# Performance work log

Hardware: AMD Instinct MI355X
Metric: run time of the kernel (lower is better)

The kernel has to match this reference:

```python
import jax, jax.numpy as jnp
import numpy as np


def setup_inputs() -> dict:
    key = jax.random.key(0)
    kx, kq, kb, kc = jax.random.split(key, 4)
    N, D = 16384, 1024
    x = jax.random.normal(kx, (N, D), dtype=jnp.float32)
    Q = jax.random.normal(kq, (D, D), dtype=jnp.float32)
    b = jax.random.normal(kb, (D,), dtype=jnp.float32)
    c = jax.random.normal(kc, (1,), dtype=jnp.float32)
    return {"x": x, "Q": Q, "b": b, "c": c}


def reference(x, Q, b, c):
    # y_i = x_i^T Q x_i + b^T x_i + c  (same math as diag(x @ Q @ x.T)
    # without materializing the NxN matrix)
    xQ = x @ Q                                # [N, D]
    quad = jnp.sum(xQ * x, axis=-1)           # [N]
    y = quad + x @ b + c                       # [N] (c broadcasts from [1])
    return y[:, None]                          # [N, 1]
```

## Files before the change

kernel.cpp:

```cpp
#include <hip/hip_runtime.h>
#include <hip/hip_bf16.h>


#define DD 1024
#define KH 256
#define KSTEP 8
#define NTT 32
#define LDS_ROW 264

typedef short v8s __attribute__((ext_vector_type(8)));
typedef float v4f __attribute__((ext_vector_type(4)));

__device__ __forceinline__ short f2b(float f) {
    union { __hip_bfloat16 h; short s; } u;
    u.h = __float2bfloat16(f);
    return u.s;
}

__global__ __launch_bounds__(512, 2)
void quad_kernel(const float* __restrict__ x, const float* __restrict__ Q,
                 const float* __restrict__ bvec, const float* __restrict__ cptr,
                 float* __restrict__ y)
{
    __shared__ short lq[2][16 * LDS_ROW];

    const int tid  = threadIdx.x;
    const int lane = tid & 63;
    const int wave = tid >> 6;
    const int quad = lane >> 4;
    const int l15  = lane & 15;

    const int seg  = blockIdx.x & 7;
    const int rblk = blockIdx.x >> 3;
    const int kq   = seg >> 1;
    const int cs   = seg & 1;

    const int row_base = rblk * 512 + wave * 64;
    const int kofs  = kq * KH;
    const int tbase = cs * NTT;

    v8s a[4][KSTEP];
    #pragma unroll
    for (int g = 0; g < 4; ++g) {
        const float* xr = x + (size_t)(row_base + g * 16 + l15) * DD + kofs + quad * 8;
        #pragma unroll
        for (int s = 0; s < KSTEP; ++s) {
            const float4 f0 = *(const float4*)(xr + s * 32);
            const float4 f1 = *(const float4*)(xr + s * 32 + 4);
            v8s t;
            t[0]=f2b(f0.x); t[1]=f2b(f0.y); t[2]=f2b(f0.z); t[3]=f2b(f0.w);
            t[4]=f2b(f1.x); t[5]=f2b(f1.y); t[6]=f2b(f1.z); t[7]=f2b(f1.w);
            a[g][s] = t;
            asm volatile("" : "+a"(a[g][s]));
        }
    }

    int s_nn[2], s_k4[2];
    #pragma unroll
    for (int i = 0; i < 2; ++i) {
        const int idx = tid + i * 512;
        s_nn[i] = idx >> 6;
        s_k4[i] = idx & 63;
    }

    float4 pf[2];
    #pragma unroll
    for (int i = 0; i < 2; ++i)
        pf[i] = *(const float4*)(Q + (size_t)(tbase * 16 + s_nn[i]) * DD + kofs + s_k4[i] * 4);

    float acc[4][4];
    #pragma unroll
    for (int g = 0; g < 4; ++g)
        #pragma unroll
        for (int r = 0; r < 4; ++r) acc[g][r] = 0.f;

    for (int t = 0; t < NTT; ++t) {
        const int tg = tbase + t;

        short* dst = &lq[t & 1][0];
        #pragma unroll
        for (int i = 0; i < 2; ++i) {
            const float4 f = pf[i];
            short4 s;
            s.x=f2b(f.x); s.y=f2b(f.y); s.z=f2b(f.z); s.w=f2b(f.w);
            *(short4*)&dst[s_nn[i] * LDS_ROW + s_k4[i] * 4] = s;
        }
        __syncthreads();

        if (t + 1 < NTT) {
            #pragma unroll
            for (int i = 0; i < 2; ++i)
                pf[i] = *(const float4*)(Q + (size_t)((tg + 1) * 16 + s_nn[i]) * DD + kofs + s_k4[i] * 4);
        }

        const int n = tg * 16 + l15;
        const float bn = (kq == 0) ? bvec[n] : 0.f;
        float xv[4][4];
        {
            const float* xc = x + (size_t)(row_base + quad * 4) * DD + n;
            #pragma unroll
            for (int g = 0; g < 4; ++g)
                #pragma unroll
                for (int r = 0; r < 4; ++r)
                    xv[g][r] = xc[(size_t)(g * 16 + r) * DD];
        }

        v4f cf[4];
        #pragma unroll
        for (int g = 0; g < 4; ++g) cf[g] = (v4f){0.f, 0.f, 0.f, 0.f};
        const short* bp = &lq[t & 1][l15 * LDS_ROW + quad * 8];
        #pragma unroll
        for (int s = 0; s < KSTEP; ++s) {
            const v8s bfrag = *(const v8s*)(bp + s * 32);
            #pragma unroll
            for (int g = 0; g < 4; ++g)
                cf[g] = __builtin_amdgcn_mfma_f32_16x16x32_bf16(a[g][s], bfrag, cf[g], 0, 0, 0);
        }

        #pragma unroll
        for (int g = 0; g < 4; ++g)
            #pragma unroll
            for (int r = 0; r < 4; ++r)
                acc[g][r] += (cf[g][r] + bn) * xv[g][r];
    }

    const float cc = (seg == 0) ? cptr[0] : 0.f;
    #pragma unroll
    for (int g = 0; g < 4; ++g) {
        #pragma unroll
        for (int r = 0; r < 4; ++r) {
            float v = acc[g][r];
            v += __shfl_xor(v, 1); v += __shfl_xor(v, 2);
            v += __shfl_xor(v, 4); v += __shfl_xor(v, 8);
            if (l15 == 0)
                atomicAdd(&y[row_base + g * 16 + quad * 4 + r], v + cc);
        }
    }
}

extern "C" void kernel_launch(void* const* d_in, const int* in_sizes, int n_in,
                              void* d_out, int out_size, void* d_ws, size_t ws_size,
                              hipStream_t stream)
{
    const float* x = (const float*)d_in[0];
    const float* Q = (const float*)d_in[1];
    const float* b = (const float*)d_in[2];
    const float* c = (const float*)d_in[3];
    float* y = (float*)d_out;

    hipMemsetAsync(y, 0, (size_t)out_size * sizeof(float), stream);
    quad_kernel<<<dim3(256), dim3(512), 0, stream>>>(x, Q, b, c, y);
}
```

Measured before the change: 155.2 us.

## Reshape block tile to 256 rows by 32 columns per round, doubling grid

Each wave now covers 32 rows instead of 64, and each round stages 32 columns of Q into LDS instead of 16, with two B fragments per k-step. The grid doubles to 512 blocks so the 256 CUs get more blocks, and the number of barrier rounds per block halves. The register footprint for the x fragments shrinks while LDS per block doubles. In exchange, Q traffic per output row rises because each block serves fewer rows.

```diff
diff --git a/kernel.cpp b/kernel.cpp
--- a/kernel.cpp
+++ b/kernel.cpp
@@ -5,7 +5,7 @@
 #define DD 1024
 #define KH 256
 #define KSTEP 8
-#define NTT 32
+#define NROUND 16
 #define LDS_ROW 264
 
 typedef short v8s __attribute__((ext_vector_type(8)));
@@ -22,7 +22,7 @@
                  const float* __restrict__ bvec, const float* __restrict__ cptr,
                  float* __restrict__ y)
 {
-    __shared__ short lq[2][16 * LDS_ROW];
+    __shared__ short lq[2][32 * LDS_ROW];
 
     const int tid  = threadIdx.x;
     const int lane = tid & 63;
@@ -35,13 +35,13 @@
     const int kq   = seg >> 1;
     const int cs   = seg & 1;
 
-    const int row_base = rblk * 512 + wave * 64;
-    const int kofs  = kq * KH;
-    const int tbase = cs * NTT;
+    const int row_base = rblk * 256 + wave * 32;
+    const int kofs     = kq * KH;
+    const int col_base = cs * 512;
 
-    v8s a[4][KSTEP];
+    v8s a[2][KSTEP];
     #pragma unroll
-    for (int g = 0; g < 4; ++g) {
+    for (int g = 0; g < 2; ++g) {
         const float* xr = x + (size_t)(row_base + g * 16 + l15) * DD + kofs + quad * 8;
         #pragma unroll
         for (int s = 0; s < KSTEP; ++s) {
@@ -55,31 +55,29 @@
         }
     }
 
-    int s_nn[2], s_k4[2];
+    int s_nn[4], s_k4[4];
     #pragma unroll
-    for (int i = 0; i < 2; ++i) {
+    for (int i = 0; i < 4; ++i) {
         const int idx = tid + i * 512;
         s_nn[i] = idx >> 6;
         s_k4[i] = idx & 63;
     }
 
-    float4 pf[2];
+    float4 pf[4];
     #pragma unroll
-    for (int i = 0; i < 2; ++i)
-        pf[i] = *(const float4*)(Q + (size_t)(tbase * 16 + s_nn[i]) * DD + kofs + s_k4[i] * 4);
+    for (int i = 0; i < 4; ++i)
+        pf[i] = *(const float4*)(Q + (size_t)(col_base + s_nn[i]) * DD + kofs + s_k4[i] * 4);
 
-    float acc[4][4];
+    float acc[2][4];
     #pragma unroll
-    for (int g = 0; g < 4; ++g)
+    for (int g = 0; g < 2; ++g)
         #pragma unroll
         for (int r = 0; r < 4; ++r) acc[g][r] = 0.f;
 
-    for (int t = 0; t < NTT; ++t) {
-        const int tg = tbase + t;
-
+    for (int t = 0; t < NROUND; ++t) {
         short* dst = &lq[t & 1][0];
         #pragma unroll
-        for (int i = 0; i < 2; ++i) {
+        for (int i = 0; i < 4; ++i) {
             const float4 f = pf[i];
             short4 s;
             s.x=f2b(f.x); s.y=f2b(f.y); s.z=f2b(f.z); s.w=f2b(f.w);
@@ -87,46 +85,55 @@
         }
         __syncthreads();
 
-        if (t + 1 < NTT) {
+        if (t + 1 < NROUND) {
             #pragma unroll
-            for (int i = 0; i < 2; ++i)
-                pf[i] = *(const float4*)(Q + (size_t)((tg + 1) * 16 + s_nn[i]) * DD + kofs + s_k4[i] * 4);
+            for (int i = 0; i < 4; ++i)
+                pf[i] = *(const float4*)(Q + (size_t)(col_base + (t + 1) * 32 + s_nn[i]) * DD + kofs + s_k4[i] * 4);
         }
 
-        const int n = tg * 16 + l15;
-        const float bn = (kq == 0) ? bvec[n] : 0.f;
-        float xv[4][4];
+        const int n0 = col_base + t * 32 + l15;
+        const float bn0 = (kq == 0) ? bvec[n0]      : 0.f;
+        const float bn1 = (kq == 0) ? bvec[n0 + 16] : 0.f;
+        float xv[2][2][4];
         {
-            const float* xc = x + (size_t)(row_base + quad * 4) * DD + n;
+            const float* xc = x + (size_t)(row_base + quad * 4) * DD + n0;
             #pragma unroll
-            for (int g = 0; g < 4; ++g)
+            for (int nt = 0; nt < 2; ++nt)
                 #pragma unroll
-                for (int r = 0; r < 4; ++r)
-                    xv[g][r] = xc[(size_t)(g * 16 + r) * DD];
+                for (int g = 0; g < 2; ++g)
+                    #pragma unroll
+                    for (int r = 0; r < 4; ++r)
+                        xv[nt][g][r] = xc[(size_t)(g * 16 + r) * DD + nt * 16];
         }
 
-        v4f cf[4];
+        v4f cf[2][2];
         #pragma unroll
-        for (int g = 0; g < 4; ++g) cf[g] = (v4f){0.f, 0.f, 0.f, 0.f};
+        for (int nt = 0; nt < 2; ++nt)
+            #pragma unroll
+            for (int g = 0; g < 2; ++g) cf[nt][g] = (v4f){0.f, 0.f, 0.f, 0.f};
         const short* bp = &lq[t & 1][l15 * LDS_ROW + quad * 8];
         #pragma unroll
         for (int s = 0; s < KSTEP; ++s) {
-            const v8s bfrag = *(const v8s*)(bp + s * 32);
+            const v8s b0 = *(const v8s*)(bp + s * 32);
+            const v8s b1 = *(const v8s*)(bp + 16 * LDS_ROW + s * 32);
             #pragma unroll
-            for (int g = 0; g < 4; ++g)
-                cf[g] = __builtin_amdgcn_mfma_f32_16x16x32_bf16(a[g][s], bfrag, cf[g], 0, 0, 0);
+            for (int g = 0; g < 2; ++g) {
+                cf[0][g] = __builtin_amdgcn_mfma_f32_16x16x32_bf16(a[g][s], b0, cf[0][g], 0, 0, 0);
+                cf[1][g] = __builtin_amdgcn_mfma_f32_16x16x32_bf16(a[g][s], b1, cf[1][g], 0, 0, 0);
+            }
         }
 
         #pragma unroll
-        for (int g = 0; g < 4; ++g)
+        for (int g = 0; g < 2; ++g)
             #pragma unroll
             for (int r = 0; r < 4; ++r)
-                acc[g][r] += (cf[g][r] + bn) * xv[g][r];
+                acc[g][r] += (cf[0][g][r] + bn0) * xv[0][g][r]
+                           + (cf[1][g][r] + bn1) * xv[1][g][r];
     }
 
     const float cc = (seg == 0) ? cptr[0] : 0.f;
     #pragma unroll
-    for (int g = 0; g < 4; ++g) {
+    for (int g = 0; g < 2; ++g) {
         #pragma unroll
         for (int r = 0; r < 4; ++r) {
             float v = acc[g][r];
@@ -149,5 +156,5 @@
     float* y = (float*)d_out;
 
     hipMemsetAsync(y, 0, (size_t)out_size * sizeof(float), stream);
-    quad_kernel<<<dim3(256), dim3(512), 0, stream>>>(x, Q, b, c, y);
+    quad_kernel<<<dim3(512), dim3(512), 0, stream>>>(x, Q, b, c, y);
 }
```

After: 152.4 us. Within noise of the previous version (-1.8%).

## Restructure to 32-row blocks with in-block K split and LDS reduction

Applied to the files above, without the earlier changes.

Each block now handles 32 rows across all of K. Its 8 waves split the work as 2 row groups by 4 K quarters, and partial MFMA results are reduced through shared memory instead of global atomics, which also removes the memset. The x values used in the epilogue come from the bf16 copies already held in registers and staged into LDS, replacing strided global loads, at some precision cost. The trade-off is two block barriers per column tile and every block streaming all of Q, which raises Q traffic per block.

```diff
diff --git a/kernel.cpp b/kernel.cpp
--- a/kernel.cpp
+++ b/kernel.cpp
@@ -3,10 +3,8 @@
 
 
 #define DD 1024
-#define KH 256
-#define KSTEP 8
-#define NTT 32
-#define LDS_ROW 264
+#define TROW 2064
+#define XROW 272
 
 typedef short v8s __attribute__((ext_vector_type(8)));
 typedef float v4f __attribute__((ext_vector_type(4)));
@@ -17,125 +15,120 @@
     return u.s;
 }
 
-__global__ __launch_bounds__(512, 2)
+__global__ __launch_bounds__(512, 4)
 void quad_kernel(const float* __restrict__ x, const float* __restrict__ Q,
                  const float* __restrict__ bvec, const float* __restrict__ cptr,
                  float* __restrict__ y)
 {
-    __shared__ short lq[2][16 * LDS_ROW];
+    __shared__ __align__(16) char  tile[16 * TROW];
+    __shared__ float parts[2][4][16][16];
+    __shared__ __align__(16) short xvb[2][32][XROW];
 
     const int tid  = threadIdx.x;
     const int lane = tid & 63;
     const int wave = tid >> 6;
     const int quad = lane >> 4;
     const int l15  = lane & 15;
+    const int kq   = wave & 3;
+    const int rg   = wave >> 2;
 
-    const int seg  = blockIdx.x & 7;
-    const int rblk = blockIdx.x >> 3;
-    const int kq   = seg >> 1;
-    const int cs   = seg & 1;
+    const int row_base = blockIdx.x * 32;
 
-    const int row_base = rblk * 512 + wave * 64;
-    const int kofs  = kq * KH;
-    const int tbase = cs * NTT;
+    const int sn = tid >> 8;
+    const int sk = tid & 255;
 
-    v8s a[4][KSTEP];
+    float4 pf[8];
     #pragma unroll
-    for (int g = 0; g < 4; ++g) {
-        const float* xr = x + (size_t)(row_base + g * 16 + l15) * DD + kofs + quad * 8;
+    for (int i = 0; i < 8; ++i)
+        pf[i] = *(const float4*)(Q + (size_t)(sn + 2 * i) * DD + sk * 4);
+
+    v8s a[8];
+    {
+        const float* xr = x + (size_t)(row_base + rg * 16 + l15) * DD + kq * 256 + quad * 8;
         #pragma unroll
-        for (int s = 0; s < KSTEP; ++s) {
+        for (int s = 0; s < 8; ++s) {
             const float4 f0 = *(const float4*)(xr + s * 32);
             const float4 f1 = *(const float4*)(xr + s * 32 + 4);
             v8s t;
             t[0]=f2b(f0.x); t[1]=f2b(f0.y); t[2]=f2b(f0.z); t[3]=f2b(f0.w);
             t[4]=f2b(f1.x); t[5]=f2b(f1.y); t[6]=f2b(f1.z); t[7]=f2b(f1.w);
-            a[g][s] = t;
-            asm volatile("" : "+a"(a[g][s]));
+            a[s] = t;
+            asm volatile("" : "+a"(a[s]));
         }
     }
 
-    int s_nn[2], s_k4[2];
-    #pragma unroll
-    for (int i = 0; i < 2; ++i) {
-        const int idx = tid + i * 512;
-        s_nn[i] = idx >> 6;
-        s_k4[i] = idx & 63;
+    if (kq == 0) {
+        char* d = (char*)&xvb[0][rg * 16 + l15][0] + quad * 16;
+        #pragma unroll
+        for (int s = 0; s < 8; ++s) *(v8s*)(d + s * 64) = a[s];
     }
 
-    float4 pf[2];
     #pragma unroll
-    for (int i = 0; i < 2; ++i)
-        pf[i] = *(const float4*)(Q + (size_t)(tbase * 16 + s_nn[i]) * DD + kofs + s_k4[i] * 4);
+    for (int i = 0; i < 8; ++i) {
+        const float4 f = pf[i];
+        short4 s4; s4.x=f2b(f.x); s4.y=f2b(f.y); s4.z=f2b(f.z); s4.w=f2b(f.w);
+        *(short4*)(tile + (sn + 2 * i) * TROW + sk * 8) = s4;
+    }
+    #pragma unroll
+    for (int i = 0; i < 8; ++i)
+        pf[i] = *(const float4*)(Q + (size_t)(16 + sn + 2 * i) * DD + sk * 4);
 
-    float acc[4][4];
-    #pragma unroll
-    for (int g = 0; g < 4; ++g)
+    __syncthreads();
+
+    const char* bp = tile + l15 * TROW + kq * 512 + quad * 16;
+    float* pw = &parts[rg][kq][quad * 4][0] + l15;
+    const int m = tid >> 4;
+    const int c = tid & 15;
+    const float* pr = &parts[m >> 4][0][m & 15][c];
+
+    float acc = 0.f;
+
+    for (int t = 0; t < 64; ++t) {
+        const float bb = bvec[t * 16 + c];
+
+        v4f cf = (v4f){0.f, 0.f, 0.f, 0.f};
         #pragma unroll
-        for (int r = 0; r < 4; ++r) acc[g][r] = 0.f;
+        for (int s = 0; s < 8; ++s) {
+            const v8s bf = *(const v8s*)(bp + s * 64);
+            cf = __builtin_amdgcn_mfma_f32_16x16x32_bf16(a[s], bf, cf, 0, 0, 0);
+        }
+        #pragma unroll
+        for (int r = 0; r < 4; ++r) pw[r * 16] = cf[r];
 
-    for (int t = 0; t < NTT; ++t) {
-        const int tg = tbase + t;
-
-        short* dst = &lq[t & 1][0];
-        #pragma unroll
-        for (int i = 0; i < 2; ++i) {
-            const float4 f = pf[i];
-            short4 s;
-            s.x=f2b(f.x); s.y=f2b(f.y); s.z=f2b(f.z); s.w=f2b(f.w);
-            *(short4*)&dst[s_nn[i] * LDS_ROW + s_k4[i] * 4] = s;
-        }
         __syncthreads();
 
-        if (t + 1 < NTT) {
+        if (t < 63) {
             #pragma unroll
-            for (int i = 0; i < 2; ++i)
-                pf[i] = *(const float4*)(Q + (size_t)((tg + 1) * 16 + s_nn[i]) * DD + kofs + s_k4[i] * 4);
+            for (int i = 0; i < 8; ++i) {
+                const float4 f = pf[i];
+                short4 s4; s4.x=f2b(f.x); s4.y=f2b(f.y); s4.z=f2b(f.z); s4.w=f2b(f.w);
+                *(short4*)(tile + (sn + 2 * i) * TROW + sk * 8) = s4;
+            }
+            if (t < 62) {
+                #pragma unroll
+                for (int i = 0; i < 8; ++i)
+                    pf[i] = *(const float4*)(Q + (size_t)((t + 2) * 16 + sn + 2 * i) * DD + sk * 4);
+            }
+        }
+        if ((t & 15) == 15 && t < 48 && kq == (t >> 4) + 1) {
+            char* d = (char*)&xvb[((t >> 4) + 1) & 1][rg * 16 + l15][0] + quad * 16;
+            #pragma unroll
+            for (int s = 0; s < 8; ++s) *(v8s*)(d + s * 64) = a[s];
         }
 
-        const int n = tg * 16 + l15;
-        const float bn = (kq == 0) ? bvec[n] : 0.f;
-        float xv[4][4];
-        {
-            const float* xc = x + (size_t)(row_base + quad * 4) * DD + n;
-            #pragma unroll
-            for (int g = 0; g < 4; ++g)
-                #pragma unroll
-                for (int r = 0; r < 4; ++r)
-                    xv[g][r] = xc[(size_t)(g * 16 + r) * DD];
-        }
+        const float cs = pr[0] + pr[256] + pr[512] + pr[768];
+        const int xo = ((t >> 4) & 1) * (32 * XROW) + m * XROW + (t & 15) * 16 + c;
+        union { unsigned u; float f; } uu;
+        uu.u = ((unsigned)(unsigned short)((const short*)xvb)[xo]) << 16;
+        acc += (cs + bb) * uu.f;
 
-        v4f cf[4];
-        #pragma unroll
-        for (int g = 0; g < 4; ++g) cf[g] = (v4f){0.f, 0.f, 0.f, 0.f};
-        const short* bp = &lq[t & 1][l15 * LDS_ROW + quad * 8];
-        #pragma unroll
-        for (int s = 0; s < KSTEP; ++s) {
-            const v8s bfrag = *(const v8s*)(bp + s * 32);
-            #pragma unroll
-            for (int g = 0; g < 4; ++g)
-                cf[g] = __builtin_amdgcn_mfma_f32_16x16x32_bf16(a[g][s], bfrag, cf[g], 0, 0, 0);
-        }
-
-        #pragma unroll
-        for (int g = 0; g < 4; ++g)
-            #pragma unroll
-            for (int r = 0; r < 4; ++r)
-                acc[g][r] += (cf[g][r] + bn) * xv[g][r];
+        __syncthreads();
     }
 
-    const float cc = (seg == 0) ? cptr[0] : 0.f;
-    #pragma unroll
-    for (int g = 0; g < 4; ++g) {
-        #pragma unroll
-        for (int r = 0; r < 4; ++r) {
-            float v = acc[g][r];
-            v += __shfl_xor(v, 1); v += __shfl_xor(v, 2);
-            v += __shfl_xor(v, 4); v += __shfl_xor(v, 8);
-            if (l15 == 0)
-                atomicAdd(&y[row_base + g * 16 + quad * 4 + r], v + cc);
-        }
-    }
+    float v = acc;
+    v += __shfl_xor(v, 1); v += __shfl_xor(v, 2);
+    v += __shfl_xor(v, 4); v += __shfl_xor(v, 8);
+    if (c == 0) y[row_base + m] = v + cptr[0];
 }
 
 extern "C" void kernel_launch(void* const* d_in, const int* in_sizes, int n_in,
@@ -148,6 +141,5 @@
     const float* c = (const float*)d_in[3];
     float* y = (float*)d_out;
 
-    hipMemsetAsync(y, 0, (size_t)out_size * sizeof(float), stream);
-    quad_kernel<<<dim3(256), dim3(512), 0, stream>>>(x, Q, b, c, y);
+    quad_kernel<<<dim3(512), dim3(512), 0, stream>>>(x, Q, b, c, y);
 }
```

Result: slower. 195.6 us (+26.0%).

## Pre-convert Q to bf16, split K across waves, and read x values from LDS

Applied to the files above, without the earlier changes.

A separate kernel now converts Q to bf16 into the workspace. The main kernel gives each block 64 rows, with each of its 8 waves owning a 128-wide K slice. Q fragments are read straight from global memory with a register double buffer, replacing the LDS staging path. Each wave writes its bf16 x fragments back to LDS as float, so the x·(xQ) dot no longer needs strided global loads. A final LDS reduction across waves replaces the memset and atomics, at the cost of an extra launch, a workspace buffer, and x values that are now bf16-rounded in the dot product.

```diff
diff --git a/kernel.cpp b/kernel.cpp
--- a/kernel.cpp
+++ b/kernel.cpp
@@ -3,10 +3,8 @@
 
 
 #define DD 1024
-#define KH 256
-#define KSTEP 8
-#define NTT 32
-#define LDS_ROW 264
+#define XSTRIDE 132
+#define XPHASE (64 * XSTRIDE)
 
 typedef short v8s __attribute__((ext_vector_type(8)));
 typedef float v4f __attribute__((ext_vector_type(4)));
@@ -16,13 +14,66 @@
     u.h = __float2bfloat16(f);
     return u.s;
 }
+__device__ __forceinline__ float b2f(short s) {
+    union { unsigned u; float f; } uu;
+    uu.u = ((unsigned)(unsigned short)s) << 16;
+    return uu.f;
+}
+
+__global__ __launch_bounds__(256, 4)
+void cvt_kernel(const float* __restrict__ Q, short* __restrict__ qb)
+{
+    const int idx = (blockIdx.x * 256 + threadIdx.x) * 4;
+    const float4 f = *(const float4*)(Q + idx);
+    short4 s4;
+    s4.x = f2b(f.x); s4.y = f2b(f.y); s4.z = f2b(f.z); s4.w = f2b(f.w);
+    *(short4*)(qb + idx) = s4;
+}
+
+#define MFMA16(A, B, C) __builtin_amdgcn_mfma_f32_16x16x32_bf16(A, B, C, 0, 0, 0)
+
+#define DUMP_XV()                                                         \
+  { _Pragma("unroll")                                                     \
+    for (int g = 0; g < 4; ++g) {                                         \
+      _Pragma("unroll")                                                   \
+      for (int s = 0; s < 4; ++s) {                                       \
+        float* d = &xvb[wave & 1][(g * 16 + l15) * XSTRIDE + s * 32 + quad * 8]; \
+        const v8s fr = a[g][s];                                           \
+        float4 lo, hi;                                                    \
+        lo.x = b2f(fr[0]); lo.y = b2f(fr[1]); lo.z = b2f(fr[2]); lo.w = b2f(fr[3]); \
+        hi.x = b2f(fr[4]); hi.y = b2f(fr[5]); hi.z = b2f(fr[6]); hi.w = b2f(fr[7]); \
+        *(float4*)d = lo; *((float4*)d + 1) = hi;                         \
+      } } }
+
+#define ROUND(BR, T)                                                      \
+  { v4f cf0 = (v4f){0,0,0,0}, cf1 = (v4f){0,0,0,0};                       \
+    v4f cf2 = (v4f){0,0,0,0}, cf3 = (v4f){0,0,0,0};                       \
+    _Pragma("unroll")                                                     \
+    for (int s = 0; s < 4; ++s) {                                         \
+      cf0 = MFMA16(a[0][s], BR[s], cf0);                                  \
+      cf1 = MFMA16(a[1][s], BR[s], cf1);                                  \
+      cf2 = MFMA16(a[2][s], BR[s], cf2);                                  \
+      cf3 = MFMA16(a[3][s], BR[s], cf3);                                  \
+    }                                                                     \
+    const float* xp = xq + ((((T) >> 3) & 1) * XPHASE) + (((T) & 7) * 16); \
+    const float bb = (wave == 0) ? bvec[(T) * 16 + l15] : 0.f;            \
+    _Pragma("unroll")                                                     \
+    for (int g = 0; g < 4; ++g) {                                         \
+      const v4f cfg = (g == 0) ? cf0 : ((g == 1) ? cf1 : ((g == 2) ? cf2 : cf3)); \
+      _Pragma("unroll")                                                   \
+      for (int r = 0; r < 4; ++r) {                                       \
+        const float xv = xp[(g * 16 + r) * XSTRIDE];                      \
+        acc[g][r] += cfg[r] * xv;                                         \
+        if (wave == 0) acc[g][r] += bb * xv;                              \
+      } } }
 
 __global__ __launch_bounds__(512, 2)
-void quad_kernel(const float* __restrict__ x, const float* __restrict__ Q,
+void quad_kernel(const float* __restrict__ x, const short* __restrict__ qb,
                  const float* __restrict__ bvec, const float* __restrict__ cptr,
                  float* __restrict__ y)
 {
-    __shared__ short lq[2][16 * LDS_ROW];
+    __shared__ __align__(16) float xvb[2][XPHASE];
+    __shared__ float yred[8][64];
 
     const int tid  = threadIdx.x;
     const int lane = tid & 63;
@@ -30,21 +81,20 @@
     const int quad = lane >> 4;
     const int l15  = lane & 15;
 
-    const int seg  = blockIdx.x & 7;
-    const int rblk = blockIdx.x >> 3;
-    const int kq   = seg >> 1;
-    const int cs   = seg & 1;
+    const int row_base = blockIdx.x * 64;
+    const int kb = wave * 128;
 
-    const int row_base = rblk * 512 + wave * 64;
-    const int kofs  = kq * KH;
-    const int tbase = cs * NTT;
+    const short* qp = qb + (size_t)l15 * DD + kb + quad * 8;
+    v8s bA[4], bB[4];
+    #pragma unroll
+    for (int s = 0; s < 4; ++s) bA[s] = *(const v8s*)(qp + s * 32);
 
-    v8s a[4][KSTEP];
+    v8s a[4][4];
     #pragma unroll
     for (int g = 0; g < 4; ++g) {
-        const float* xr = x + (size_t)(row_base + g * 16 + l15) * DD + kofs + quad * 8;
+        const float* xr = x + (size_t)(row_base + g * 16 + l15) * DD + kb + quad * 8;
         #pragma unroll
-        for (int s = 0; s < KSTEP; ++s) {
+        for (int s = 0; s < 4; ++s) {
             const float4 f0 = *(const float4*)(xr + s * 32);
             const float4 f1 = *(const float4*)(xr + s * 32 + 4);
             v8s t;
@@ -55,18 +105,8 @@
         }
     }
 
-    int s_nn[2], s_k4[2];
-    #pragma unroll
-    for (int i = 0; i < 2; ++i) {
-        const int idx = tid + i * 512;
-        s_nn[i] = idx >> 6;
-        s_k4[i] = idx & 63;
-    }
-
-    float4 pf[2];
-    #pragma unroll
-    for (int i = 0; i < 2; ++i)
-        pf[i] = *(const float4*)(Q + (size_t)(tbase * 16 + s_nn[i]) * DD + kofs + s_k4[i] * 4);
+    if (wave == 0) DUMP_XV();
+    __syncthreads();
 
     float acc[4][4];
     #pragma unroll
@@ -74,67 +114,40 @@
         #pragma unroll
         for (int r = 0; r < 4; ++r) acc[g][r] = 0.f;
 
-    for (int t = 0; t < NTT; ++t) {
-        const int tg = tbase + t;
+    const float* xq = &xvb[0][0] + quad * 4 * XSTRIDE + l15;
 
-        short* dst = &lq[t & 1][0];
+    for (int t = 0; t < 64; t += 2) {
+        if ((t & 7) == 0) {
+            if (t) __syncthreads();
+            if (wave == (t >> 3) + 1) DUMP_XV();
+        }
+        qp += 16 * DD;
         #pragma unroll
-        for (int i = 0; i < 2; ++i) {
-            const float4 f = pf[i];
-            short4 s;
-            s.x=f2b(f.x); s.y=f2b(f.y); s.z=f2b(f.z); s.w=f2b(f.w);
-            *(short4*)&dst[s_nn[i] * LDS_ROW + s_k4[i] * 4] = s;
+        for (int s = 0; s < 4; ++s) bB[s] = *(const v8s*)(qp + s * 32);
+        ROUND(bA, t);
+        qp += 16 * DD;
+        if (t + 2 < 64) {
+            #pragma unroll
+            for (int s = 0; s < 4; ++s) bA[s] = *(const v8s*)(qp + s * 32);
         }
-        __syncthreads();
-
-        if (t + 1 < NTT) {
-            #pragma unroll
-            for (int i = 0; i < 2; ++i)
-                pf[i] = *(const float4*)(Q + (size_t)((tg + 1) * 16 + s_nn[i]) * DD + kofs + s_k4[i] * 4);
-        }
-
-        const int n = tg * 16 + l15;
-        const float bn = (kq == 0) ? bvec[n] : 0.f;
-        float xv[4][4];
-        {
-            const float* xc = x + (size_t)(row_base + quad * 4) * DD + n;
-            #pragma unroll
-            for (int g = 0; g < 4; ++g)
-                #pragma unroll
-                for (int r = 0; r < 4; ++r)
-                    xv[g][r] = xc[(size_t)(g * 16 + r) * DD];
-        }
-
-        v4f cf[4];
-        #pragma unroll
-        for (int g = 0; g < 4; ++g) cf[g] = (v4f){0.f, 0.f, 0.f, 0.f};
-        const short* bp = &lq[t & 1][l15 * LDS_ROW + quad * 8];
-        #pragma unroll
-        for (int s = 0; s < KSTEP; ++s) {
-            const v8s bfrag = *(const v8s*)(bp + s * 32);
-            #pragma unroll
-            for (int g = 0; g < 4; ++g)
-                cf[g] = __builtin_amdgcn_mfma_f32_16x16x32_bf16(a[g][s], bfrag, cf[g], 0, 0, 0);
-        }
-
-        #pragma unroll
-        for (int g = 0; g < 4; ++g)
-            #pragma unroll
-            for (int r = 0; r < 4; ++r)
-                acc[g][r] += (cf[g][r] + bn) * xv[g][r];
+        ROUND(bB, t + 1);
     }
 
-    const float cc = (seg == 0) ? cptr[0] : 0.f;
     #pragma unroll
-    for (int g = 0; g < 4; ++g) {
+    for (int g = 0; g < 4; ++g)
         #pragma unroll
         for (int r = 0; r < 4; ++r) {
             float v = acc[g][r];
             v += __shfl_xor(v, 1); v += __shfl_xor(v, 2);
             v += __shfl_xor(v, 4); v += __shfl_xor(v, 8);
             if (l15 == 0)
-                atomicAdd(&y[row_base + g * 16 + quad * 4 + r], v + cc);
+                yred[wave][g * 16 + quad * 4 + r] = v;
         }
+    __syncthreads();
+    if (tid < 64) {
+        float s = yred[0][tid] + yred[1][tid] + yred[2][tid] + yred[3][tid]
+                + yred[4][tid] + yred[5][tid] + yred[6][tid] + yred[7][tid];
+        y[row_base + tid] = s + cptr[0];
     }
 }
 
@@ -147,7 +160,8 @@
     const float* b = (const float*)d_in[2];
     const float* c = (const float*)d_in[3];
     float* y = (float*)d_out;
+    short* qb = (short*)d_ws;
 
-    hipMemsetAsync(y, 0, (size_t)out_size * sizeof(float), stream);
-    quad_kernel<<<dim3(256), dim3(512), 0, stream>>>(x, Q, b, c, y);
+    cvt_kernel<<<dim3(1024), dim3(256), 0, stream>>>(Q, qb);
+    quad_kernel<<<dim3(256), dim3(512), 0, stream>>>(x, qb, b, c, y);
 }
```

Result: slower. 225.6 us (+45.3%).
